# Performance work log

Measured on AMD Instinct MI355X. Metric: run time of the kernel, lower is better.

Reference implementation:

```python
import jax, jax.numpy as jnp
import numpy as np

B, T, D = 64, 8192, 16   # batch, time, state dim
H = 128                  # recurr_size
HID = (256, 256)         # MLP hidden sizes
OUT = 1                  # output_dim
F = D + 1                # features + weight channel


def setup_inputs() -> dict:
    key = jax.random.key(0)
    ks = jax.random.split(key, 12)
    s = lambda k, shp: jax.random.normal(k, shp, jnp.float32) * 0.05
    return {
        "particles": jax.random.normal(ks[0], (B, T, D), jnp.float32),
        "weights": jax.random.uniform(ks[1], (B, T), jnp.float32),
        # GRU params: packed [r|z|n] gates; input dense has no bias (flax GRUCell),
        # hidden dense has bias.
        "Wi": s(ks[2], (F, 3 * H)),
        "Wh": s(ks[3], (H, 3 * H)),
        "bh": jnp.zeros((3 * H,), jnp.float32),
        # MLP decoder params
        "W1": s(ks[4], (H, HID[0])), "b1": jnp.zeros((HID[0],), jnp.float32),
        "W2": s(ks[5], (HID[0], HID[1])), "b2": jnp.zeros((HID[1],), jnp.float32),
        "W3": s(ks[6], (HID[1], OUT)), "b3": jnp.zeros((OUT,), jnp.float32),
        # log_std param, initialized with ones (init_log_std default)
        "log_std": jnp.ones((OUT,), jnp.float32),
    }


def _gru_last(inputs, Wi, Wh, bh):
    """Run GRU over time (axis 1 of [B,T,F]); return final hidden state [B,H].
    Equivalent to taking encoding at the last timestep."""
    h0 = jnp.zeros((inputs.shape[0], H), inputs.dtype)

    def step(h, x_t):  # x_t: [B,F]
        gi = x_t @ Wi              # [B,3H], no input bias (flax GRUCell)
        gh = h @ Wh + bh           # [B,3H]
        ir, iz, inn = jnp.split(gi, 3, axis=-1)
        hr, hz, hn = jnp.split(gh, 3, axis=-1)
        r = jax.nn.sigmoid(ir + hr)
        z = jax.nn.sigmoid(iz + hz)
        n = jnp.tanh(inn + r * hn)
        h_new = (1.0 - z) * n + z * h
        return h_new, None

    xs = jnp.swapaxes(inputs, 0, 1)  # [T,B,F]
    h_last, _ = jax.lax.scan(step, h0, xs)
    return h_last


def reference(particles, weights, Wi, Wh, bh, W1, b1, W2, b2, W3, b3, log_std):
    features = particles  # feature_fn = identity
    inputs = jnp.concatenate([features, weights[..., None]], axis=-1)  # [B,T,F]
    enc = _gru_last(inputs, Wi, Wh, bh)  # [B,H] == encoding at last timestep
    x = jax.nn.relu(enc @ W1 + b1)
    x = jax.nn.relu(x @ W2 + b2)
    mean = x @ W3 + b3  # [B,OUT]
    return mean, log_std
```

## Files before the change

kernel.cpp:

```cpp
#include <hip/hip_runtime.h>
#include <hip/hip_bf16.h>
#include <hip/hip_fp8.h>

#define B 64
#define T 8192
#define D 16
#define H 128
#define F 17
#define NTHREADS 512
#define CHUNK 32
#define XSTR 40
#define GSTR 516

typedef _Float16 half_t;
typedef _Float16 f16x8 __attribute__((ext_vector_type(8)));
typedef float f32x4 __attribute__((ext_vector_type(4)));
typedef int i32x8 __attribute__((ext_vector_type(8)));

#define MFMA(a, b, c) __builtin_amdgcn_mfma_f32_16x16x32_f16((a), (b), (c), 0, 0, 0)
#define MFMAS(a, b, c) \
  __builtin_amdgcn_mfma_scale_f32_16x16x128_f8f6f4((a), (b), (c), 0, 0, 0, 0x7F7F7F7F, 0, 0x7F7F7F7F)

__device__ __forceinline__ float fast_rcp(float x) {
#if __has_builtin(__builtin_amdgcn_rcpf)
  return __builtin_amdgcn_rcpf(x);
#else
  return 1.0f / x;
#endif
}
__device__ __forceinline__ float fast_exp2(float x) {
#if __has_builtin(__builtin_amdgcn_exp2f)
  return __builtin_amdgcn_exp2f(x);
#else
  return exp2f(x);
#endif
}
__device__ __forceinline__ unsigned char f32_to_e4m3(float f) {
  __hip_fp8_e4m3 q(f);
  return __builtin_bit_cast(unsigned char, q);
}

#define GSTEP(RB, WB, TT)                                                    \
  do {                                                                       \
    const f32x4 gv = *(const f32x4*)(gi_lds + ((TT) & 31) * GSTR + jj * 4);  \
    const i32x8 a8 = *(const i32x8*)((RB) + mg * 32);                        \
    f32x4 ar = {gv[0], gv[0], gv[0], gv[0]};                                 \
    f32x4 az = {gv[1], gv[1], gv[1], gv[1]};                                 \
    f32x4 an = {bn2, bn2, bn2, bn2};                                         \
    ar = MFMAS(a8, wb_r, ar);                                                \
    az = MFMAS(a8, wb_z, az);                                                \
    an = MFMAS(a8, wb_n, an);                                                \
    float rr = fast_rcp(1.0f + fast_exp2(-ar[0]));                           \
    float zz = fast_rcp(1.0f + fast_exp2(-az[0]));                           \
    float pre = fmaf(rr, an[0], gv[2]);                                      \
    pre = fminf(fmaxf(pre, -40.0f), 40.0f);                                  \
    float e = fast_exp2(-pre);                                               \
    float nn = (1.0f - e) * fast_rcp(1.0f + e);                              \
    hreg = fmaf(zz, hreg - nn, nn);                       \
    if (mg == 0) (WB)[jj] = f32_to_e4m3(hreg);                               \
    __syncthreads();                                                         \
  } while (0)

__global__ __launch_bounds__(NTHREADS, 1)
void policy_gru_kernel(const float* __restrict__ particles,
                       const float* __restrict__ weights,
                       const float* __restrict__ Wi, const float* __restrict__ Wh,
                       const float* __restrict__ bh,
                       const float* __restrict__ W1, const float* __restrict__ b1,
                       const float* __restrict__ W2, const float* __restrict__ b2,
                       const float* __restrict__ W3, const float* __restrict__ b3,
                       const float* __restrict__ log_std,
                       float* __restrict__ out)
{
  __shared__ __align__(32) unsigned char hb8[2][H];
  __shared__ __align__(16) half_t xs[CHUNK * XSTR];
  __shared__ __align__(16) float gi_lds[CHUNK * GSTR];
  __shared__ float sg[NTHREADS];
  __shared__ float red[8];

  const int tid = threadIdx.x;
  const int b   = blockIdx.x;
  const int l   = tid & 63;
  const int w   = tid >> 6;
  const int mg  = l >> 4;
  const int jn  = l & 15;
  const int jj  = w * 16 + jn;

  const float L1 = 1.4426950408889634f;
  const float L2 = 2.0f * L1;

  auto wload8 = [&](int gate) -> i32x8 {
    const float sc  = (gate == 2) ? L2 : L1;
    const int   col = gate * H + jj;
    i32x8 v;
    #pragma unroll
    for (int r = 0; r < 8; ++r) {
      unsigned int word = 0;
      #pragma unroll
      for (int byt = 0; byt < 4; ++byt) {
        const int k = mg * 32 + r * 4 + byt;
        word |= ((unsigned int)f32_to_e4m3(Wh[k * 384 + col] * sc)) << (8 * byt);
      }
      v[r] = (int)word;
    }
    return v;
  };
  const i32x8 wb_r = wload8(0), wb_z = wload8(1), wb_n = wload8(2);
  const float bn2 = bh[256 + jj] * L2;

  auto wiload = [&](int gate) -> f16x8 {
    f16x8 v;
    const float sc  = (gate == 2) ? L2 : L1;
    const int   col = gate * H + jj;
    #pragma unroll
    for (int i = 0; i < 8; ++i) {
      const int k = mg * 8 + i;
      v[i] = (half_t)(k < F ? Wi[k * 384 + col] * sc : 0.0f);
    }
    return v;
  };
  const f16x8 wiR = wiload(0), wiZ = wiload(1), wiN = wiload(2);
  const float br = bh[jj] * L1, bz = bh[128 + jj] * L1;

  const int e0 = tid, e1 = tid + NTHREADS;
  float xr0 = 0.f, xr1 = 0.f;
  auto xfetch = [&](int t0) {
    auto ld = [&](int e) -> float {
      const int tau = e / F, f = e % F;
      int t = t0 + tau; if (t > T - 1) t = T - 1;
      return (f < D) ? particles[((size_t)b * T + t) * D + f]
                     : weights[(size_t)b * T + t];
    };
    xr0 = ld(e0);
    if (e1 < CHUNK * F) xr1 = ld(e1);
  };
  auto xstage = [&]() {
    xs[(e0 / F) * XSTR + (e0 % F)] = (half_t)xr0;
    if (e1 < CHUNK * F) xs[(e1 / F) * XSTR + (e1 % F)] = (half_t)xr1;
  };

  auto gi_compute = [&]() {
    f16x8 aX0 = *(const f16x8*)(xs + (jn     ) * XSTR + mg * 8);
    f16x8 aX1 = *(const f16x8*)(xs + (jn + 16) * XSTR + mg * 8);
    f32x4 cr0 = {br, br, br, br}, cz0 = {bz, bz, bz, bz}, cn0 = {0.f,0.f,0.f,0.f};
    f32x4 cr1 = cr0, cz1 = cz0, cn1 = cn0;
    cr0 = MFMA(aX0, wiR, cr0); cz0 = MFMA(aX0, wiZ, cz0); cn0 = MFMA(aX0, wiN, cn0);
    cr1 = MFMA(aX1, wiR, cr1); cz1 = MFMA(aX1, wiZ, cz1); cn1 = MFMA(aX1, wiN, cn1);
    #pragma unroll
    for (int r = 0; r < 4; ++r) {
      const int t0r = mg * 4 + r;
      f32x4 v0 = {cr0[r], cz0[r], cn0[r], 0.f};
      *(f32x4*)(gi_lds + t0r * GSTR + jj * 4) = v0;
      const int t1r = t0r + 16;
      f32x4 v1 = {cr1[r], cz1[r], cn1[r], 0.f};
      *(f32x4*)(gi_lds + t1r * GSTR + jj * 4) = v1;
    }
  };

  float hreg = 0.0f;
  if (tid < H) { hb8[0][tid] = 0; hb8[1][tid] = 0; }
  for (int i = tid; i < CHUNK * XSTR; i += NTHREADS) xs[i] = (half_t)0.f;
  xfetch(0);
  __syncthreads();
  xstage();
  xfetch(CHUNK);
  __syncthreads();
  gi_compute();
  __syncthreads();

  for (int t0 = 0; t0 < T; t0 += CHUNK) {
    for (int tt = 0; tt < CHUNK; tt += 2) {
      GSTEP(hb8[0], hb8[1], tt);
      GSTEP(hb8[1], hb8[0], tt + 1);
    }
    if (t0 + CHUNK < T) {
      xstage();
      xfetch(t0 + 2 * CHUNK);
      __syncthreads();
      gi_compute();
      __syncthreads();
    }
  }

  if (mg == 0) sg[jj] = hreg;
  __syncthreads();

  float a1 = 0.0f;
  if (tid < 256) {
    a1 = b1[tid];
    #pragma unroll 4
    for (int k = 0; k < H; ++k) a1 = fmaf(sg[k], W1[k * 256 + tid], a1);
    a1 = fmaxf(a1, 0.0f);
    sg[256 + tid] = a1;
  }
  __syncthreads();

  float a2 = 0.0f;
  if (tid < 256) {
    a2 = b2[tid];
    #pragma unroll 4
    for (int k = 0; k < 256; ++k) a2 = fmaf(sg[256 + k], W2[k * 256 + tid], a2);
    a2 = fmaxf(a2, 0.0f);
    a2 *= W3[tid];
  }
  #pragma unroll
  for (int off = 32; off > 0; off >>= 1) a2 += __shfl_down(a2, off, 64);
  if (tid < 256 && (tid & 63) == 0) red[tid >> 6] = a2;
  __syncthreads();
  if (tid == 0) {
    out[b] = red[0] + red[1] + red[2] + red[3] + b3[0];
    if (b == 0) out[B] = log_std[0];
  }
}

extern "C" void kernel_launch(void* const* d_in, const int* in_sizes, int n_in,
                              void* d_out, int out_size, void* d_ws, size_t ws_size,
                              hipStream_t stream) {
  const float* particles = (const float*)d_in[0];
  const float* weights   = (const float*)d_in[1];
  const float* Wi      = (const float*)d_in[2];
  const float* Wh      = (const float*)d_in[3];
  const float* bh      = (const float*)d_in[4];
  const float* W1      = (const float*)d_in[5];
  const float* b1      = (const float*)d_in[6];
  const float* W2      = (const float*)d_in[7];
  const float* b2      = (const float*)d_in[8];
  const float* W3      = (const float*)d_in[9];
  const float* b3      = (const float*)d_in[10];
  const float* log_std = (const float*)d_in[11];

  policy_gru_kernel<<<dim3(B), dim3(NTHREADS), 0, stream>>>(
      particles, weights, Wi, Wh, bh, W1, b1, W2, b2, W3, b3, log_std,
      (float*)d_out);
}
```

Baseline: 2.584 ms.

## Pack two batch rows per block and ping-pong MFMA and gate phases

```diff
diff --git a/kernel.cpp b/kernel.cpp
--- a/kernel.cpp
+++ b/kernel.cpp
@@ -7,13 +7,14 @@
 #define D 16
 #define H 128
 #define F 17
-#define NTHREADS 512
+#define NTH 1024
 #define CHUNK 32
 #define XSTR 40
-#define GSTR 516
+#define GSTRH 528
 
 typedef _Float16 half_t;
 typedef _Float16 f16x8 __attribute__((ext_vector_type(8)));
+typedef _Float16 f16x4 __attribute__((ext_vector_type(4)));
 typedef float f32x4 __attribute__((ext_vector_type(4)));
 typedef int i32x8 __attribute__((ext_vector_type(8)));
 
@@ -40,28 +41,7 @@
   return __builtin_bit_cast(unsigned char, q);
 }
 
-#define GSTEP(RB, WB, TT)                                                    \
-  do {                                                                       \
-    const f32x4 gv = *(const f32x4*)(gi_lds + ((TT) & 31) * GSTR + jj * 4);  \
-    const i32x8 a8 = *(const i32x8*)((RB) + mg * 32);                        \
-    f32x4 ar = {gv[0], gv[0], gv[0], gv[0]};                                 \
-    f32x4 az = {gv[1], gv[1], gv[1], gv[1]};                                 \
-    f32x4 an = {bn2, bn2, bn2, bn2};                                         \
-    ar = MFMAS(a8, wb_r, ar);                                                \
-    az = MFMAS(a8, wb_z, az);                                                \
-    an = MFMAS(a8, wb_n, an);                                                \
-    float rr = fast_rcp(1.0f + fast_exp2(-ar[0]));                           \
-    float zz = fast_rcp(1.0f + fast_exp2(-az[0]));                           \
-    float pre = fmaf(rr, an[0], gv[2]);                                      \
-    pre = fminf(fmaxf(pre, -40.0f), 40.0f);                                  \
-    float e = fast_exp2(-pre);                                               \
-    float nn = (1.0f - e) * fast_rcp(1.0f + e);                              \
-    hreg = fmaf(zz, hreg - nn, nn);                       \
-    if (mg == 0) (WB)[jj] = f32_to_e4m3(hreg);                               \
-    __syncthreads();                                                         \
-  } while (0)
-
-__global__ __launch_bounds__(NTHREADS, 1)
+__global__ __launch_bounds__(NTH, 1)
 void policy_gru_kernel(const float* __restrict__ particles,
                        const float* __restrict__ weights,
                        const float* __restrict__ Wi, const float* __restrict__ Wh,
@@ -72,19 +52,24 @@
                        const float* __restrict__ log_std,
                        float* __restrict__ out)
 {
-  __shared__ __align__(32) unsigned char hb8[2][H];
-  __shared__ __align__(16) half_t xs[CHUNK * XSTR];
-  __shared__ __align__(16) float gi_lds[CHUNK * GSTR];
-  __shared__ float sg[NTHREADS];
-  __shared__ float red[8];
-
-  const int tid = threadIdx.x;
-  const int b   = blockIdx.x;
-  const int l   = tid & 63;
-  const int w   = tid >> 6;
-  const int mg  = l >> 4;
-  const int jn  = l & 15;
-  const int jj  = w * 16 + jn;
+  __shared__ __align__(16) unsigned char hb8[2][H];
+  __shared__ __align__(16) half_t xs[2][CHUNK * XSTR];
+  __shared__ __align__(16) half_t gi_lds[2][CHUNK * GSTRH];
+  __shared__ float red[2][8];
+
+  const int tid  = threadIdx.x;
+  const int grp  = tid >> 9;
+  const int gtid = tid & 511;
+  const int b    = blockIdx.x * 2 + grp;
+  const int l    = tid & 63;
+  const int w    = gtid >> 6;
+  const int mg   = l >> 4;
+  const int jn   = l & 15;
+  const int jj   = w * 16 + jn;
+
+  unsigned char* hbp = hb8[grp];
+  half_t* xsp = xs[grp];
+  half_t* gip = gi_lds[grp];
 
   const float L1 = 1.4426950408889634f;
   const float L2 = 2.0f * L1;
@@ -122,7 +107,7 @@
   const f16x8 wiR = wiload(0), wiZ = wiload(1), wiN = wiload(2);
   const float br = bh[jj] * L1, bz = bh[128 + jj] * L1;
 
-  const int e0 = tid, e1 = tid + NTHREADS;
+  const int e0 = gtid, e1 = gtid + 512;
   float xr0 = 0.f, xr1 = 0.f;
   auto xfetch = [&](int t0) {
     auto ld = [&](int e) -> float {
@@ -135,13 +120,13 @@
     if (e1 < CHUNK * F) xr1 = ld(e1);
   };
   auto xstage = [&]() {
-    xs[(e0 / F) * XSTR + (e0 % F)] = (half_t)xr0;
-    if (e1 < CHUNK * F) xs[(e1 / F) * XSTR + (e1 % F)] = (half_t)xr1;
+    xsp[(e0 / F) * XSTR + (e0 % F)] = (half_t)xr0;
+    if (e1 < CHUNK * F) xsp[(e1 / F) * XSTR + (e1 % F)] = (half_t)xr1;
   };
 
   auto gi_compute = [&]() {
-    f16x8 aX0 = *(const f16x8*)(xs + (jn     ) * XSTR + mg * 8);
-    f16x8 aX1 = *(const f16x8*)(xs + (jn + 16) * XSTR + mg * 8);
+    f16x8 aX0 = *(const f16x8*)(xsp + (jn     ) * XSTR + mg * 8);
+    f16x8 aX1 = *(const f16x8*)(xsp + (jn + 16) * XSTR + mg * 8);
     f32x4 cr0 = {br, br, br, br}, cz0 = {bz, bz, bz, bz}, cn0 = {0.f,0.f,0.f,0.f};
     f32x4 cr1 = cr0, cz1 = cz0, cn1 = cn0;
     cr0 = MFMA(aX0, wiR, cr0); cz0 = MFMA(aX0, wiZ, cz0); cn0 = MFMA(aX0, wiN, cn0);
@@ -149,17 +134,44 @@
     #pragma unroll
     for (int r = 0; r < 4; ++r) {
       const int t0r = mg * 4 + r;
-      f32x4 v0 = {cr0[r], cz0[r], cn0[r], 0.f};
-      *(f32x4*)(gi_lds + t0r * GSTR + jj * 4) = v0;
+      *(f16x4*)(gip + t0r * GSTRH + jj * 4) =
+          f16x4{(half_t)cr0[r], (half_t)cz0[r], (half_t)cn0[r], (half_t)0.f};
       const int t1r = t0r + 16;
-      f32x4 v1 = {cr1[r], cz1[r], cn1[r], 0.f};
-      *(f32x4*)(gi_lds + t1r * GSTR + jj * 4) = v1;
+      *(f16x4*)(gip + t1r * GSTRH + jj * 4) =
+          f16x4{(half_t)cr1[r], (half_t)cz1[r], (half_t)cn1[r], (half_t)0.f};
     }
   };
 
+  const f32x4 zc = {0.f, 0.f, 0.f, 0.f};
+  f32x4 ar = zc, az = zc, an = zc;
+  f16x4 gv = {};
   float hreg = 0.0f;
-  if (tid < H) { hb8[0][tid] = 0; hb8[1][tid] = 0; }
-  for (int i = tid; i < CHUNK * XSTR; i += NTHREADS) xs[i] = (half_t)0.f;
+
+  auto mfma_phase = [&](int t) {
+    if ((t & 31) == 0 && t > 0) gi_compute();
+    const i32x8 a8 = *(const i32x8*)(hbp + mg * 32);
+    ar = MFMAS(a8, wb_r, zc);
+    az = MFMAS(a8, wb_z, zc);
+    an = MFMAS(a8, wb_n, zc);
+    gv = *(const f16x4*)(gip + (t & 31) * GSTRH + jj * 4);
+  };
+
+  auto gates_phase = [&](int t) {
+    float sr = ar[0] + (float)gv[0];
+    float sz = az[0] + (float)gv[1];
+    float rr = fast_rcp(1.0f + fast_exp2(-sr));
+    float zz = fast_rcp(1.0f + fast_exp2(-sz));
+    float pre = fmaf(rr, an[0] + bn2, (float)gv[2]);
+    pre = fmaxf(pre, -120.0f);
+    float e = fast_exp2(-pre);
+    float nn = (1.0f - e) * fast_rcp(1.0f + e);
+    hreg = fmaf(zz, hreg - nn, nn);
+    if (mg == 0) hbp[jj] = f32_to_e4m3(hreg);
+    if ((t & 31) == 31) { xstage(); xfetch(t + 1 + CHUNK); }
+  };
+
+  if (gtid < H) hbp[gtid] = 0;
+  for (int i = gtid; i < CHUNK * XSTR; i += 512) xsp[i] = (half_t)0.f;
   xfetch(0);
   __syncthreads();
   xstage();
@@ -168,47 +180,43 @@
   gi_compute();
   __syncthreads();
 
-  for (int t0 = 0; t0 < T; t0 += CHUNK) {
-    for (int tt = 0; tt < CHUNK; tt += 2) {
-      GSTEP(hb8[0], hb8[1], tt);
-      GSTEP(hb8[1], hb8[0], tt + 1);
-    }
-    if (t0 + CHUNK < T) {
-      xstage();
-      xfetch(t0 + 2 * CHUNK);
-      __syncthreads();
-      gi_compute();
-      __syncthreads();
-    }
-  }
-
+  for (int t = 0; t < T; ++t) {
+    if (grp == 0) mfma_phase(t); else if (t > 0) gates_phase(t - 1);
+    __syncthreads();
+    if (grp == 0) gates_phase(t); else mfma_phase(t);
+    __syncthreads();
+  }
+  if (grp == 1) gates_phase(T - 1);
+  __syncthreads();
+
+  float* sg = (float*)gi_lds[grp];
   if (mg == 0) sg[jj] = hreg;
   __syncthreads();
 
   float a1 = 0.0f;
-  if (tid < 256) {
-    a1 = b1[tid];
+  if (gtid < 256) {
+    a1 = b1[gtid];
     #pragma unroll 4
-    for (int k = 0; k < H; ++k) a1 = fmaf(sg[k], W1[k * 256 + tid], a1);
+    for (int k = 0; k < H; ++k) a1 = fmaf(sg[k], W1[k * 256 + gtid], a1);
     a1 = fmaxf(a1, 0.0f);
-    sg[256 + tid] = a1;
+    sg[256 + gtid] = a1;
   }
   __syncthreads();
 
   float a2 = 0.0f;
-  if (tid < 256) {
-    a2 = b2[tid];
+  if (gtid < 256) {
+    a2 = b2[gtid];
     #pragma unroll 4
-    for (int k = 0; k < 256; ++k) a2 = fmaf(sg[256 + k], W2[k * 256 + tid], a2);
+    for (int k = 0; k < 256; ++k) a2 = fmaf(sg[256 + k], W2[k * 256 + gtid], a2);
     a2 = fmaxf(a2, 0.0f);
-    a2 *= W3[tid];
+    a2 *= W3[gtid];
   }
   #pragma unroll
   for (int off = 32; off > 0; off >>= 1) a2 += __shfl_down(a2, off, 64);
-  if (tid < 256 && (tid & 63) == 0) red[tid >> 6] = a2;
-  __syncthreads();
-  if (tid == 0) {
-    out[b] = red[0] + red[1] + red[2] + red[3] + b3[0];
+  if (gtid < 256 && (gtid & 63) == 0) red[grp][gtid >> 6] = a2;
+  __syncthreads();
+  if (gtid == 0) {
+    out[b] = red[grp][0] + red[grp][1] + red[grp][2] + red[grp][3] + b3[0];
     if (b == 0) out[B] = log_std[0];
   }
 }
@@ -229,7 +237,7 @@
   const float* b3      = (const float*)d_in[10];
   const float* log_std = (const float*)d_in[11];
 
-  policy_gru_kernel<<<dim3(B), dim3(NTHREADS), 0, stream>>>(
+  policy_gru_kernel<<<dim3(B / 2), dim3(NTH), 0, stream>>>(
       particles, weights, Wi, Wh, bh, W1, b1, W2, b2, W3, b3, log_std,
       (float*)d_out);
 }
```

After: 4.927 ms. 1.91x slower.
